# Optimization experiments

Measured on AMD Instinct MI355X. Metric: run time of the kernel, lower is better.

Reference implementation:

```python
import jax, jax.numpy as jnp
import numpy as np

EPS = 1e-5  # BatchNorm2d default eps


def _binarize_ste(x):
    """Forward: sign(x). Backward: hardtanh STE (grad 1 where |x|<=1, else 0)."""
    xc = jnp.clip(x, -1.0, 1.0)
    return xc + jax.lax.stop_gradient(jnp.sign(x) - xc)


def setup_inputs() -> dict:
    key = jax.random.key(0)
    k1, k2, k3, k4 = jax.random.split(key, 4)
    x = jax.random.normal(k1, (32, 256, 32, 32), dtype=jnp.float32)
    # BatchNorm affine params (affine=True)
    gamma = 1.0 + 0.1 * jax.random.normal(k2, (256,), dtype=jnp.float32)
    beta = 0.1 * jax.random.normal(k3, (256,), dtype=jnp.float32)
    # Conv weight, OIHW, bias=False
    W = 0.05 * jax.random.normal(k4, (256, 256, 3, 3), dtype=jnp.float32)
    return {"x": x, "gamma": gamma, "beta": beta, "W": W}


def reference(x, gamma, beta, W):
    # BatchNorm2d, training-mode batch statistics over (N, H, W) per channel
    mean = jnp.mean(x, axis=(0, 2, 3), keepdims=True)
    var = jnp.var(x, axis=(0, 2, 3), keepdims=True)
    xn = (x - mean) * jax.lax.rsqrt(var + EPS)
    xn = xn * gamma[None, :, None, None] + beta[None, :, None, None]
    # Conv2d_1w1a: binarize activations and weights (sign fwd / STE bwd), then conv
    a = _binarize_ste(xn)
    wb = _binarize_ste(W)
    out = jax.lax.conv_general_dilated(
        a, wb,
        window_strides=(1, 1),
        padding=((1, 1), (1, 1)),
        dimension_numbers=("NCHW", "OIHW", "NCHW"),
    )
    return out
```

## Files before the change

kernel.cpp:

```cpp
#include <hip/hip_runtime.h>
#include <hip/hip_bf16.h>


#define NIMG 32
#define C    256
#define K    256

typedef int v4i  __attribute__((ext_vector_type(4)));
typedef int v16i __attribute__((ext_vector_type(16)));

#define AHT_IMG 295936
#define AHT_KB  36992
#define AHT_ROW 1088


__global__ __launch_bounds__(256) void k_stats_packw(
    const float* __restrict__ x, const float* __restrict__ W,
    double2* __restrict__ partials, char* __restrict__ wfrag) {
  int bx = blockIdx.x;
  int tid = threadIdx.x;
  if (bx >= 2048) {
    int k = bx - 2048, c = tid;
    const float* src = W + ((size_t)k * 256 + c) * 9;
    char* dst = wfrag + (size_t)(c >> 4) * 4096 + k * 16 + (c & 15);
    #pragma unroll
    for (int t = 0; t < 9; ++t)
      dst[(size_t)t * 65536] = (src[t] > 0.0f) ? (char)1 : (char)-1;
    return;
  }
  int c = bx >> 3, grp = bx & 7;
  double s = 0.0, sq = 0.0;
  #pragma unroll
  for (int ni = 0; ni < 4; ++ni) {
    int n = grp * 4 + ni;
    const float* p = x + (size_t)n * (C * 1024) + (size_t)c * 1024;
    float4 v = ((const float4*)p)[tid];
    s += (double)v.x + (double)v.y + (double)v.z + (double)v.w;
    sq += (double)v.x * v.x + (double)v.y * v.y
        + (double)v.z * v.z + (double)v.w * v.w;
  }
  for (int o = 32; o > 0; o >>= 1) {
    s += __shfl_down(s, o);
    sq += __shfl_down(sq, o);
  }
  __shared__ double ls[4], lq[4];
  if ((tid & 63) == 0) { ls[tid >> 6] = s; lq[tid >> 6] = sq; }
  __syncthreads();
  if (tid == 0) {
    double2 r;
    r.x = ls[0] + ls[1] + ls[2] + ls[3];
    r.y = lq[0] + lq[1] + lq[2] + lq[3];
    partials[c * 8 + grp] = r;
  }
}

__global__ __launch_bounds__(256) void k_packa_i8(
    const float* __restrict__ x, const double2* __restrict__ partials,
    const float* __restrict__ gamma, const float* __restrict__ beta,
    char* __restrict__ aHT) {
  __shared__ float lf[32 * 257];
  __shared__ float lthr[256];
  __shared__ unsigned lfl[256];
  int y = blockIdx.x, n = blockIdx.y, tid = threadIdx.x;

  {
    double S = 0.0, Q = 0.0;
    #pragma unroll
    for (int g = 0; g < 8; ++g) {
      double2 p = partials[tid * 8 + g];
      S += p.x; Q += p.y;
    }
    const double N = 32768.0;
    double mean = S / N;
    double var = Q / N - mean * mean;
    double rs = 1.0 / sqrt(var + 1e-5);
    double gm = (double)gamma[tid];
    double bt = (double)beta[tid];
    float t;
    unsigned flip;
    if (gm == 0.0) {
      t = (bt > 0.0) ? -3.0e38f : 3.0e38f;
      flip = 0u;
    } else {
      t = (float)(mean - bt / (rs * gm));
      flip = (gm < 0.0) ? 1u : 0u;
    }
    lthr[tid] = t;
    lfl[tid] = flip;
  }

  #pragma unroll
  for (int it = 0; it < 8; ++it) {
    int c = it * 32 + (tid >> 3), q = tid & 7;
    float4 v = *(const float4*)(x + (size_t)n * 262144 + (size_t)c * 1024
                                + y * 32 + q * 4);
    lf[(q * 4 + 0) * 257 + c] = v.x;
    lf[(q * 4 + 1) * 257 + c] = v.y;
    lf[(q * 4 + 2) * 257 + c] = v.z;
    lf[(q * 4 + 3) * 257 + c] = v.w;
  }
  __syncthreads();
  int xl = tid & 31, cb = tid >> 5;
  unsigned wds[8];
  #pragma unroll
  for (int g = 0; g < 8; ++g) {
    unsigned wv = 0;
    #pragma unroll
    for (int jj = 0; jj < 4; ++jj) {
      int c = cb * 32 + g * 4 + jj;
      float v = lf[xl * 257 + c];
      unsigned bit = ((v > lthr[c]) ? 1u : 0u) ^ lfl[c];
      unsigned byte = bit ? 0x01u : 0xFFu;
      wv |= byte << (8 * jj);
    }
    wds[g] = wv;
  }
  char* dst = aHT + ((size_t)n * 8 + cb) * AHT_KB
            + (size_t)(y + 1) * AHT_ROW + (size_t)(xl + 1) * 32;
  uint4 u0, u1;
  u0.x = wds[0]; u0.y = wds[1]; u0.z = wds[2]; u0.w = wds[3];
  u1.x = wds[4]; u1.y = wds[5]; u1.z = wds[6]; u1.w = wds[7];
  *(uint4*)dst = u0;
  *((uint4*)dst + 1) = u1;

  uint4 z; z.x = 0; z.y = 0; z.z = 0; z.w = 0;
  if (xl < 2) {
    char* hz = aHT + ((size_t)n * 8 + cb) * AHT_KB
             + (size_t)(y + 1) * AHT_ROW + (size_t)(xl * 33) * 32;
    *(uint4*)hz = z;
    *((uint4*)hz + 1) = z;
  }
  if (y == 0 || y == 31) {
    int row = (y == 0) ? 0 : 33;
    for (int idx = tid; idx < 272; idx += 256) {
      int kb = idx / 34, xx = idx % 34;
      char* hz = aHT + ((size_t)n * 8 + kb) * AHT_KB
               + (size_t)row * AHT_ROW + (size_t)xx * 32;
      *(uint4*)hz = z;
      *((uint4*)hz + 1) = z;
    }
  }
}

__global__ __launch_bounds__(512) void k_conv_mfma(
    const char* __restrict__ aHT, const char* __restrict__ wfrag,
    float* __restrict__ out) {
  int tid = threadIdx.x;
  int lane = tid & 63, w = tid >> 6;
  int nh = w & 3, mb = w >> 2;
  int bx = blockIdx.x;
  int lb = (bx & 7) * 32 + (bx >> 3);
  int n = lb >> 3, ys = lb & 7;
  int yw = ys * 4 + mb * 2;
  int xl = lane & 31, hi = lane >> 5;

  const char* abT = aHT + (size_t)n * AHT_IMG + (size_t)(xl + 1) * 32 + hi * 16;
  const char* wB = wfrag + hi * 4096 + (nh * 64 + xl) * 16;

  v16i a00 = {0}, a01 = {0}, a10 = {0}, a11 = {0};
  v4i cA00, cA01, cA10, cA11, nA00, nA01, nA10, nA11;
  v4i cB0, cB1, cB2, cB3, nB0, nB1, nB2, nB3;

  {
    const char* ab = abT + (size_t)yw * AHT_ROW - 32;
    cA00 = *(const v4i*)(ab);
    cA01 = *(const v4i*)(ab + AHT_ROW);
    cA10 = *(const v4i*)(ab + AHT_KB);
    cA11 = *(const v4i*)(ab + AHT_KB + AHT_ROW);
    cB0 = *(const v4i*)(wB);
    cB1 = *(const v4i*)(wB + 512);
    cB2 = *(const v4i*)(wB + 8192);
    cB3 = *(const v4i*)(wB + 8192 + 512);
  }

  for (int p = 0; p < 36; ++p) {
    if (p < 35) {
      int pp = p + 1;
      int tt = pp >> 2;
      int kb0 = (pp & 3) * 2;
      int dy = tt / 3 - 1, dx = tt % 3 - 1;
      const char* ab = abT + (size_t)kb0 * AHT_KB
                     + (size_t)(yw + dy + 1) * AHT_ROW + dx * 32;
      nA00 = *(const v4i*)(ab);
      nA01 = *(const v4i*)(ab + AHT_ROW);
      nA10 = *(const v4i*)(ab + AHT_KB);
      nA11 = *(const v4i*)(ab + AHT_KB + AHT_ROW);
      const char* wp2 = wB + (size_t)pp * 16384;
      nB0 = *(const v4i*)(wp2);
      nB1 = *(const v4i*)(wp2 + 512);
      nB2 = *(const v4i*)(wp2 + 8192);
      nB3 = *(const v4i*)(wp2 + 8192 + 512);
    }
    a00 = __builtin_amdgcn_mfma_i32_32x32x32_i8(cA00, cB0, a00, 0, 0, 0);
    a01 = __builtin_amdgcn_mfma_i32_32x32x32_i8(cA00, cB1, a01, 0, 0, 0);
    a10 = __builtin_amdgcn_mfma_i32_32x32x32_i8(cA01, cB0, a10, 0, 0, 0);
    a11 = __builtin_amdgcn_mfma_i32_32x32x32_i8(cA01, cB1, a11, 0, 0, 0);
    a00 = __builtin_amdgcn_mfma_i32_32x32x32_i8(cA10, cB2, a00, 0, 0, 0);
    a01 = __builtin_amdgcn_mfma_i32_32x32x32_i8(cA10, cB3, a01, 0, 0, 0);
    a10 = __builtin_amdgcn_mfma_i32_32x32x32_i8(cA11, cB2, a10, 0, 0, 0);
    a11 = __builtin_amdgcn_mfma_i32_32x32x32_i8(cA11, cB3, a11, 0, 0, 0);
    if (p < 35) {
      cA00 = nA00; cA01 = nA01; cA10 = nA10; cA11 = nA11;
      cB0 = nB0; cB1 = nB1; cB2 = nB2; cB3 = nB3;
    }
    __builtin_amdgcn_s_barrier();
  }

  size_t ob0 = (size_t)n * 262144 + (size_t)(nh * 64 + xl) * 1024
             + (size_t)yw * 32 + 4 * hi;
  #pragma unroll
  for (int r = 0; r < 2; ++r) {
    #pragma unroll
    for (int nb = 0; nb < 2; ++nb) {
      v16i av = (r == 0) ? (nb == 0 ? a00 : a01) : (nb == 0 ? a10 : a11);
      float* obp = out + ob0 + (size_t)nb * 32768 + r * 32;
      #pragma unroll
      for (int q = 0; q < 4; ++q) {
        float4 f;
        f.x = (float)av[q * 4 + 0];
        f.y = (float)av[q * 4 + 1];
        f.z = (float)av[q * 4 + 2];
        f.w = (float)av[q * 4 + 3];
        *(float4*)(obp + 8 * q) = f;
      }
    }
  }
}


__global__ __launch_bounds__(256) void k_stats_part_fb(
    const float* __restrict__ x, double2* __restrict__ partials) {
  int grp = blockIdx.x;
  int c = blockIdx.y;
  int tid = threadIdx.x;
  double s = 0.0, sq = 0.0;
  #pragma unroll
  for (int ni = 0; ni < 4; ++ni) {
    int n = grp * 4 + ni;
    const float* p = x + (size_t)n * (C * 1024) + (size_t)c * 1024;
    float4 v = ((const float4*)p)[tid];
    s += (double)v.x + (double)v.y + (double)v.z + (double)v.w;
    sq += (double)v.x * v.x + (double)v.y * v.y
        + (double)v.z * v.z + (double)v.w * v.w;
  }
  for (int o = 32; o > 0; o >>= 1) {
    s += __shfl_down(s, o);
    sq += __shfl_down(sq, o);
  }
  __shared__ double ls[4], lq[4];
  if ((tid & 63) == 0) { ls[tid >> 6] = s; lq[tid >> 6] = sq; }
  __syncthreads();
  if (tid == 0) {
    double2 r;
    r.x = ls[0] + ls[1] + ls[2] + ls[3];
    r.y = lq[0] + lq[1] + lq[2] + lq[3];
    partials[c * 8 + grp] = r;
  }
}

__global__ __launch_bounds__(256) void k_packw_corr_final(
    const float* __restrict__ W, const double2* __restrict__ partials,
    const float* __restrict__ gamma, const float* __restrict__ beta,
    unsigned* __restrict__ wp, int* __restrict__ corr,
    unsigned* __restrict__ zp, float* __restrict__ t_out,
    unsigned* __restrict__ flip_out) {
  int bk = blockIdx.x;
  int tid = threadIdx.x;
  if (bk == 256) {
    int c = tid;
    double S = 0.0, Q = 0.0;
    #pragma unroll
    for (int g = 0; g < 8; ++g) {
      double2 p = partials[c * 8 + g];
      S += p.x; Q += p.y;
    }
    const double N = 32768.0;
    double mean = S / N;
    double var = Q / N - mean * mean;
    double rs = 1.0 / sqrt(var + 1e-5);
    double g = (double)gamma[c];
    double b = (double)beta[c];
    float t;
    unsigned flip;
    if (g == 0.0) {
      t = (b > 0.0) ? -3.0e38f : 3.0e38f;
      flip = 0u;
    } else {
      t = (float)(mean - b / (rs * g));
      flip = (g < 0.0) ? 1u : 0u;
    }
    t_out[c] = t;
    flip_out[c] = flip;
    return;
  }
  int k = bk;
  __shared__ unsigned lw[72];
  float w[9];
  const float* src = W + (size_t)k * 2304 + (size_t)tid * 9;
  #pragma unroll
  for (int t = 0; t < 9; ++t) w[t] = src[t];
  int lane = tid & 63, wv = tid >> 6;
  #pragma unroll
  for (int t = 0; t < 9; ++t) {
    unsigned long long m = __ballot(w[t] > 0.0f);
    if (lane == 0) {
      lw[t * 8 + 2 * wv] = (unsigned)m;
      lw[t * 8 + 2 * wv + 1] = (unsigned)(m >> 32);
    }
  }
  __syncthreads();
  if (tid < 72) wp[(size_t)k * 72 + tid] = lw[tid];
  if (tid >= 128 && tid < 144) {
    int cls = tid - 128;
    int sum = 0;
    #pragma unroll
    for (int t = 0; t < 9; ++t) {
      int dy = t / 3 - 1, dx = t % 3 - 1;
      bool inv = (((cls & 1) && dx == -1) || ((cls & 2) && dx == 1) ||
                  ((cls & 4) && dy == -1) || ((cls & 8) && dy == 1));
      if (inv) {
        #pragma unroll
        for (int j = 0; j < 8; ++j) sum += __popc(lw[t * 8 + j]);
      }
    }
    corr[k * 16 + cls] = sum;
  }
  if (bk == 0 && tid >= 192 && tid < 200) zp[tid - 192] = 0u;
}

__global__ __launch_bounds__(256) void k_packa_bits(
    const float* __restrict__ x, const float* __restrict__ t,
    const unsigned* __restrict__ flip, unsigned* __restrict__ ap) {
  int n = blockIdx.y;
  int p0 = blockIdx.x * 64;
  int pix = threadIdx.x & 63;
  int q = threadIdx.x >> 6;
  unsigned w0 = 0, w1 = 0;
  const float* xb = x + (size_t)n * (C * 1024) + p0 + pix;
  #pragma unroll
  for (int i = 0; i < 64; ++i) {
    int c = q * 64 + i;
    float tv = t[c];
    unsigned fl = flip[c];
    float v = xb[(size_t)c * 1024];
    unsigned bit = ((v > tv) ? 1u : 0u) ^ fl;
    if (i < 32) w0 |= bit << i;
    else        w1 |= bit << (i - 32);
  }
  uint2 st; st.x = w0; st.y = w1;
  *(uint2*)(ap + ((size_t)n * 1024 + p0 + pix) * 8 + q * 2) = st;
}

__global__ __launch_bounds__(256) void k_conv_pop(
    const unsigned* __restrict__ ap, const unsigned* __restrict__ wp,
    const int* __restrict__ corr, const unsigned* __restrict__ zp,
    float* __restrict__ out) {
  int n = blockIdx.z;
  int ystrip = blockIdx.y;
  int kc = blockIdx.x;
  int tid = threadIdx.x;
  int lane = tid & 63;
  int wave = tid >> 6;
  int y = ystrip * 8 + wave * 2 + (lane >> 5);
  int xx = lane & 31;
  int cls = (xx == 0 ? 1 : 0) | (xx == 31 ? 2 : 0) |
            (y == 0 ? 4 : 0) | (y == 31 ? 8 : 0);
  uint4 a0[9], a1[9];
  int nv = 0;
  const uint4* zp4 = (const uint4*)zp;
  #pragma unroll
  for (int t = 0; t < 9; ++t) {
    int dy = t / 3 - 1, dx = t % 3 - 1;
    int cy = y + dy, cx = xx + dx;
    bool valid = (cy >= 0) & (cy < 32) & (cx >= 0) & (cx < 32);
    nv += valid ? 1 : 0;
    const uint4* pa = valid
        ? (const uint4*)(ap + (((size_t)n * 32 + cy) * 32 + cx) * 8)
        : zp4;
    a0[t] = pa[0];
    a1[t] = pa[1];
  }
  int bias = nv << 8;
  float* ob = out + (size_t)n * (K * 1024) + (size_t)y * 32 + xx;
  for (int kk = 0; kk < 16; ++kk) {
    int k = kc * 16 + kk;
    const uint4* wq = (const uint4*)(wp + (size_t)k * 72);
    int s0 = 0, s1 = 0, s2 = 0, s3 = 0, s4 = 0, s5 = 0, s6 = 0, s7 = 0;
    #pragma unroll
    for (int t = 0; t < 9; ++t) {
      uint4 wa = wq[t * 2];
      uint4 wb = wq[t * 2 + 1];
      s0 += __popc(a0[t].x ^ wa.x);
      s1 += __popc(a0[t].y ^ wa.y);
      s2 += __popc(a0[t].z ^ wa.z);
      s3 += __popc(a0[t].w ^ wa.w);
      s4 += __popc(a1[t].x ^ wb.x);
      s5 += __popc(a1[t].y ^ wb.y);
      s6 += __popc(a1[t].z ^ wb.z);
      s7 += __popc(a1[t].w ^ wb.w);
    }
    int S = ((s0 + s1) + (s2 + s3)) + ((s4 + s5) + (s6 + s7));
    int tot = corr[(k << 4) + cls] - S;
    ob[(size_t)k * 1024] = (float)(bias + 2 * tot);
  }
}


extern "C" void kernel_launch(void* const* d_in, const int* in_sizes, int n_in,
                              void* d_out, int out_size, void* d_ws, size_t ws_size,
                              hipStream_t stream) {
  const float* x = (const float*)d_in[0];
  const float* gamma = (const float*)d_in[1];
  const float* beta = (const float*)d_in[2];
  const float* W = (const float*)d_in[3];
  float* out = (float*)d_out;
  char* ws = (char*)d_ws;

  const size_t NEED = 655360 + (size_t)NIMG * AHT_IMG;
  if (ws_size >= NEED) {
    double2* partials = (double2*)(ws + 4096);
    char* wfrag = ws + 36864;
    char* aHT = ws + 655360;

    k_stats_packw<<<2304, 256, 0, stream>>>(x, W, partials, wfrag);
    k_packa_i8<<<dim3(32, 32), 256, 0, stream>>>(x, partials, gamma, beta, aHT);
    k_conv_mfma<<<256, 512, 0, stream>>>(aHT, wfrag, out);
  } else {
    float* t = (float*)ws;
    unsigned* flip = (unsigned*)(ws + 1024);
    unsigned* wp = (unsigned*)(ws + 4096);
    unsigned* zp = (unsigned*)(ws + 77824);
    int* corr = (int*)(ws + 78336);
    double2* partials = (double2*)(ws + 98304);
    unsigned* ap = (unsigned*)(ws + 131072);

    k_stats_part_fb<<<dim3(8, 256), 256, 0, stream>>>(x, partials);
    k_packw_corr_final<<<257, 256, 0, stream>>>(W, partials, gamma, beta,
                                                wp, corr, zp, t, flip);
    k_packa_bits<<<dim3(16, 32), 256, 0, stream>>>(x, t, flip, ap);
    k_conv_pop<<<dim3(16, 4, 32), 256, 0, stream>>>(ap, wp, corr, zp, out);
  }
}
```

Measured before the change: 50.79 us.

## Stage activation tiles in double-buffered LDS shared across conv waves

The A-operand activation fragments were loaded directly from global memory by every wave, so the four waves sharing the same rows reloaded identical data. Now each wave loads one 16-byte piece per step into a double-buffered shared-memory tile, and all waves read their MFMA A fragments from LDS. This cuts redundant global loads per block, but adds LDS writes and reads plus an lgkmcnt wait before each barrier.

```diff
diff --git a/kernel.cpp b/kernel.cpp
--- a/kernel.cpp
+++ b/kernel.cpp
@@ -145,65 +145,84 @@
 __global__ __launch_bounds__(512) void k_conv_mfma(
     const char* __restrict__ aHT, const char* __restrict__ wfrag,
     float* __restrict__ out) {
+  __shared__ uint4 As4[1024];
+  char* As = (char*)As4;
   int tid = threadIdx.x;
   int lane = tid & 63, w = tid >> 6;
   int nh = w & 3, mb = w >> 2;
   int bx = blockIdx.x;
   int lb = (bx & 7) * 32 + (bx >> 3);
   int n = lb >> 3, ys = lb & 7;
-  int yw = ys * 4 + mb * 2;
+  int y0 = ys * 4;
+  int yw = y0 + mb * 2;
   int xl = lane & 31, hi = lane >> 5;
 
-  const char* abT = aHT + (size_t)n * AHT_IMG + (size_t)(xl + 1) * 32 + hi * 16;
+  int sr = w >> 1, skb = w & 1;
+  int sp = lane & 31, sh = lane >> 5;
+  const char* aBase = aHT + (size_t)n * AHT_IMG;
+  unsigned aDst = (unsigned)(w * 1024 + lane * 16);
+
   const char* wB = wfrag + hi * 4096 + (nh * 64 + xl) * 16;
 
+  unsigned aRd = (unsigned)(mb * 4096 + lane * 16);
+
   v16i a00 = {0}, a01 = {0}, a10 = {0}, a11 = {0};
-  v4i cA00, cA01, cA10, cA11, nA00, nA01, nA10, nA11;
+  v4i sA;
   v4i cB0, cB1, cB2, cB3, nB0, nB1, nB2, nB3;
 
   {
-    const char* ab = abT + (size_t)yw * AHT_ROW - 32;
-    cA00 = *(const v4i*)(ab);
-    cA01 = *(const v4i*)(ab + AHT_ROW);
-    cA10 = *(const v4i*)(ab + AHT_KB);
-    cA11 = *(const v4i*)(ab + AHT_KB + AHT_ROW);
+    const char* asrc = aBase + (size_t)skb * AHT_KB
+                     + (size_t)(y0 + sr) * AHT_ROW + (size_t)sp * 32 + sh * 16;
+    sA = *(const v4i*)asrc;
+    *(v4i*)(As + aDst) = sA;
     cB0 = *(const v4i*)(wB);
     cB1 = *(const v4i*)(wB + 512);
     cB2 = *(const v4i*)(wB + 8192);
     cB3 = *(const v4i*)(wB + 8192 + 512);
   }
+  asm volatile("s_waitcnt lgkmcnt(0)" ::: "memory");
+  __builtin_amdgcn_s_barrier();
+  asm volatile("" ::: "memory");
 
   for (int p = 0; p < 36; ++p) {
+    unsigned cur = (p & 1) ? 8192u : 0u;
+    unsigned nxt = 8192u - cur;
     if (p < 35) {
       int pp = p + 1;
       int tt = pp >> 2;
       int kb0 = (pp & 3) * 2;
       int dy = tt / 3 - 1, dx = tt % 3 - 1;
-      const char* ab = abT + (size_t)kb0 * AHT_KB
-                     + (size_t)(yw + dy + 1) * AHT_ROW + dx * 32;
-      nA00 = *(const v4i*)(ab);
-      nA01 = *(const v4i*)(ab + AHT_ROW);
-      nA10 = *(const v4i*)(ab + AHT_KB);
-      nA11 = *(const v4i*)(ab + AHT_KB + AHT_ROW);
+      const char* asrc = aBase + (size_t)(kb0 + skb) * AHT_KB
+                       + (size_t)(y0 + 1 + dy + sr) * AHT_ROW
+                       + (size_t)(sp + 1 + dx) * 32 + sh * 16;
+      sA = *(const v4i*)asrc;
       const char* wp2 = wB + (size_t)pp * 16384;
       nB0 = *(const v4i*)(wp2);
       nB1 = *(const v4i*)(wp2 + 512);
       nB2 = *(const v4i*)(wp2 + 8192);
       nB3 = *(const v4i*)(wp2 + 8192 + 512);
     }
-    a00 = __builtin_amdgcn_mfma_i32_32x32x32_i8(cA00, cB0, a00, 0, 0, 0);
-    a01 = __builtin_amdgcn_mfma_i32_32x32x32_i8(cA00, cB1, a01, 0, 0, 0);
-    a10 = __builtin_amdgcn_mfma_i32_32x32x32_i8(cA01, cB0, a10, 0, 0, 0);
-    a11 = __builtin_amdgcn_mfma_i32_32x32x32_i8(cA01, cB1, a11, 0, 0, 0);
-    a00 = __builtin_amdgcn_mfma_i32_32x32x32_i8(cA10, cB2, a00, 0, 0, 0);
-    a01 = __builtin_amdgcn_mfma_i32_32x32x32_i8(cA10, cB3, a01, 0, 0, 0);
-    a10 = __builtin_amdgcn_mfma_i32_32x32x32_i8(cA11, cB2, a10, 0, 0, 0);
-    a11 = __builtin_amdgcn_mfma_i32_32x32x32_i8(cA11, cB3, a11, 0, 0, 0);
+    {
+      v4i A00 = *(const v4i*)(As + cur + aRd);
+      v4i A01 = *(const v4i*)(As + cur + aRd + 1024);
+      v4i A10 = *(const v4i*)(As + cur + aRd + 2048);
+      v4i A11 = *(const v4i*)(As + cur + aRd + 3072);
+      a00 = __builtin_amdgcn_mfma_i32_32x32x32_i8(A00, cB0, a00, 0, 0, 0);
+      a01 = __builtin_amdgcn_mfma_i32_32x32x32_i8(A00, cB1, a01, 0, 0, 0);
+      a10 = __builtin_amdgcn_mfma_i32_32x32x32_i8(A10, cB0, a10, 0, 0, 0);
+      a11 = __builtin_amdgcn_mfma_i32_32x32x32_i8(A10, cB1, a11, 0, 0, 0);
+      a00 = __builtin_amdgcn_mfma_i32_32x32x32_i8(A01, cB2, a00, 0, 0, 0);
+      a01 = __builtin_amdgcn_mfma_i32_32x32x32_i8(A01, cB3, a01, 0, 0, 0);
+      a10 = __builtin_amdgcn_mfma_i32_32x32x32_i8(A11, cB2, a10, 0, 0, 0);
+      a11 = __builtin_amdgcn_mfma_i32_32x32x32_i8(A11, cB3, a11, 0, 0, 0);
+    }
     if (p < 35) {
-      cA00 = nA00; cA01 = nA01; cA10 = nA10; cA11 = nA11;
+      *(v4i*)(As + nxt + aDst) = sA;
       cB0 = nB0; cB1 = nB1; cB2 = nB2; cB3 = nB3;
     }
+    asm volatile("s_waitcnt lgkmcnt(0)" ::: "memory");
     __builtin_amdgcn_s_barrier();
+    asm volatile("" ::: "memory");
   }
 
   size_t ob0 = (size_t)n * 262144 + (size_t)(nh * 64 + xl) * 1024
```

After: 58.36 us. +14.9%, slower.
